# Kernel tuning notes

Hardware: AMD Instinct MI355X
Metric: run time of the kernel (lower is better)

The kernel has to match this reference:

```python
import jax, jax.numpy as jnp
import numpy as np
import math

EMBED = 1024
HEADS = 16
HEAD_DIM = 64
HIDDEN = 4 * EMBED
EPS = 1e-5


def setup_inputs() -> dict:
    key = jax.random.key(0)
    ks = jax.random.split(key, 12)
    B, T, C = 2, 2048, EMBED
    s = 0.02
    return {
        "x": jax.random.normal(ks[0], (B, T, C), jnp.float32),
        "ln1_g": jnp.ones((C,), jnp.float32),
        "ln1_b": jnp.zeros((C,), jnp.float32),
        "qkv_w": jax.random.normal(ks[1], (C, 3 * C), jnp.float32) * s,
        "qkv_b": jnp.zeros((3 * C,), jnp.float32),
        "out_w": jax.random.normal(ks[2], (C, C), jnp.float32) * s,
        "out_b": jnp.zeros((C,), jnp.float32),
        "ln2_g": jnp.ones((C,), jnp.float32),
        "ln2_b": jnp.zeros((C,), jnp.float32),
        "fc1_w": jax.random.normal(ks[3], (C, HIDDEN), jnp.float32) * s,
        "fc1_b": jnp.zeros((HIDDEN,), jnp.float32),
        "fc2_w": jax.random.normal(ks[4], (HIDDEN, C), jnp.float32) * s,
        "fc2_b": jnp.zeros((C,), jnp.float32),
    }


def _layernorm(x, g, b):
    mu = jnp.mean(x, axis=-1, keepdims=True)
    var = jnp.var(x, axis=-1, keepdims=True)
    return (x - mu) * jax.lax.rsqrt(var + EPS) * g + b


def _attention(x, qkv_w, qkv_b, out_w, out_b):
    B, T, C = x.shape
    qkv = x @ qkv_w + qkv_b  # [B,T,3C]
    q, k, v = jnp.split(qkv, 3, axis=-1)
    # [B,H,T,hd]
    def heads(t):
        return t.reshape(B, T, HEADS, HEAD_DIM).transpose(0, 2, 1, 3)
    q, k, v = heads(q), heads(k), heads(v)
    scale = 1.0 / math.sqrt(HEAD_DIM)
    attn = jnp.einsum('bhqd,bhkd->bhqk', q, k) * scale
    causal = jnp.triu(jnp.ones((T, T), bool), k=1)
    attn = jnp.where(causal, -jnp.inf, attn)
    attn = jax.nn.softmax(attn, axis=-1)
    out = jnp.einsum('bhqk,bhkd->bhqd', attn, v)
    out = out.transpose(0, 2, 1, 3).reshape(B, T, C)
    return out @ out_w + out_b


def reference(x, ln1_g, ln1_b, qkv_w, qkv_b, out_w, out_b, ln2_g, ln2_b, fc1_w, fc1_b, fc2_w, fc2_b):
    x = x + _attention(_layernorm(x, ln1_g, ln1_b), qkv_w, qkv_b, out_w, out_b)
    h = _layernorm(x, ln2_g, ln2_b)
    h = jax.nn.gelu(h @ fc1_w + fc1_b, approximate=False) @ fc2_w + fc2_b
    return x + h
```

## Files before the change

### kernel.cpp

```cpp
#include <hip/hip_runtime.h>
#include <hip/hip_bf16.h>
#include <math.h>

typedef float f32x4 __attribute__((ext_vector_type(4)));
typedef __bf16 bf16x8 __attribute__((ext_vector_type(8)));
typedef __hip_bfloat16 bf16;

constexpr int T_SEQ = 2048;
constexpr int C_EMB = 1024;
constexpr int N_HEAD = 16;
constexpr int D_HEAD = 64;
constexpr int BATCH = 2;
constexpr int M_ROWS = BATCH * T_SEQ;
constexpr int HIDDEN_DIM = 4096;

static __device__ __forceinline__ f32x4 zero4() {
  f32x4 z; z[0] = 0.f; z[1] = 0.f; z[2] = 0.f; z[3] = 0.f; return z;
}

static __device__ __forceinline__ void gl_lds16(const bf16* g, bf16* l) {
  __builtin_amdgcn_global_load_lds(
      (const __attribute__((address_space(1))) unsigned int*)g,
      (__attribute__((address_space(3))) unsigned int*)l, 16, 0, 0);
}

static __device__ __forceinline__ int swz_row(int l) {
  return 2 * (l >> 3) + (((l >> 2) ^ (l >> 5)) & 1);
}
static __device__ __forceinline__ int swz_col16(int l) {
  return (l & 3) ^ ((l >> 3) & 3);
}
static __device__ __forceinline__ int swz_rd(int rr, int g) {
  return (rr >> 1) * 64 + ((((rr & 1) ^ ((rr >> 3) & 1))) << 5) +
         (((g ^ ((rr >> 1) & 3)) & 3) << 3);
}

__global__ __launch_bounds__(256) void ln_kernel(const float* __restrict__ x,
                                                 const float* __restrict__ gamma,
                                                 const float* __restrict__ beta,
                                                 bf16* __restrict__ out) {
  int row = blockIdx.x;
  const float* xr = x + (size_t)row * C_EMB;
  int t = threadIdx.x;
  float4 v = *(const float4*)&xr[t * 4];
  float s = v.x + v.y + v.z + v.w;
  float ss = v.x * v.x + v.y * v.y + v.z * v.z + v.w * v.w;
#pragma unroll
  for (int off = 32; off > 0; off >>= 1) {
    s += __shfl_down(s, off, 64);
    ss += __shfl_down(ss, off, 64);
  }
  __shared__ float sbuf[8];
  int w = t >> 6;
  if ((t & 63) == 0) { sbuf[w] = s; sbuf[4 + w] = ss; }
  __syncthreads();
  s = sbuf[0] + sbuf[1] + sbuf[2] + sbuf[3];
  ss = sbuf[4] + sbuf[5] + sbuf[6] + sbuf[7];
  float mu = s * (1.0f / C_EMB);
  float var = ss * (1.0f / C_EMB) - mu * mu;
  float rstd = rsqrtf(var + 1e-5f);
  float4 g4 = *(const float4*)&gamma[t * 4];
  float4 b4 = *(const float4*)&beta[t * 4];
  bf16* orow = out + (size_t)row * C_EMB + t * 4;
  orow[0] = __float2bfloat16((v.x - mu) * rstd * g4.x + b4.x);
  orow[1] = __float2bfloat16((v.y - mu) * rstd * g4.y + b4.y);
  orow[2] = __float2bfloat16((v.z - mu) * rstd * g4.z + b4.z);
  orow[3] = __float2bfloat16((v.w - mu) * rstd * g4.w + b4.w);
}

__global__ __launch_bounds__(256) void cast_transpose(const float* __restrict__ src,
                                                      bf16* __restrict__ dst,
                                                      int K, int N) {
  __shared__ float tile[32][33];
  int n0 = blockIdx.x * 32, k0 = blockIdx.y * 32;
  int tx = threadIdx.x & 31, ty = threadIdx.x >> 5;
#pragma unroll
  for (int i = 0; i < 4; ++i)
    tile[ty + 8 * i][tx] = src[(size_t)(k0 + ty + 8 * i) * N + n0 + tx];
  __syncthreads();
#pragma unroll
  for (int i = 0; i < 4; ++i)
    dst[(size_t)(n0 + ty + 8 * i) * K + k0 + tx] = __float2bfloat16(tile[tx][ty + 8 * i]);
}

__global__ __launch_bounds__(256) void transpose_v(const bf16* __restrict__ V,
                                                   bf16* __restrict__ Vt) {
  int tt = blockIdx.x, bh = blockIdx.y;
  __shared__ bf16 tile[64][72];
  const bf16* src = V + ((size_t)bh * T_SEQ + tt * 64) * 64;
  int t = threadIdx.x;
  for (int idx = t; idx < 512; idx += 256) {
    int r = idx >> 3, c = (idx & 7) * 8;
    *(int4*)&tile[r][c] = *(const int4*)&src[r * 64 + c];
  }
  __syncthreads();
  bf16* dst = Vt + ((size_t)bh * 64) * T_SEQ + tt * 64;
  for (int idx = t; idx < 512; idx += 256) {
    int d = idx >> 3, c = (idx & 7) * 8;
    union { bf16 h[8]; int4 v; } u;
#pragma unroll
    for (int j = 0; j < 8; ++j) u.h[j] = tile[c + j][d];
    *(int4*)&dst[(size_t)d * T_SEQ + c] = u.v;
  }
}

template <int EPI>
__global__ __launch_bounds__(256) void gemm128(
    const bf16* __restrict__ A, const bf16* __restrict__ Bt,
    const float* __restrict__ bias, int M, int N, int K, int ksplit,
    float* __restrict__ out_f32, const float* __restrict__ res,
    bf16* __restrict__ out_b16,
    bf16* __restrict__ q_out, bf16* __restrict__ k_out, bf16* __restrict__ v_out,
    float* __restrict__ part0, float* __restrict__ part1) {
  __shared__ bf16 Alds[2][128 * 32];
  __shared__ bf16 Blds[2][128 * 32];

  int gx = gridDim.x, nwg = gx * gridDim.y;
  int flat = blockIdx.y * gx + blockIdx.x;
  int swz = (flat & 7) * (nwg >> 3) + (flat >> 3);
  int bx = swz % gx, by = swz / gx;

  int m0 = by * 128, n0 = bx * 128;
  int t = threadIdx.x;
  int w = t >> 6, lane = t & 63, g = lane >> 4, r16 = lane & 15;
  int w_m = (w >> 1) * 64, w_n = (w & 1) * 64;

  f32x4 acc[4][4];
#pragma unroll
  for (int i = 0; i < 4; ++i)
#pragma unroll
    for (int j = 0; j < 4; ++j) acc[i][j] = zero4();

  int srow = swz_row(lane);
  int scol = swz_col16(lane) * 8;
  int chunk0 = w * 2, chunk1 = w * 2 + 1;

  int klen = K / ksplit;
  int kbeg = blockIdx.z * klen;
  int NT = klen / 32;

  const bf16* gA0 = A + (size_t)(m0 + chunk0 * 16 + srow) * K + kbeg + scol;
  const bf16* gA1 = A + (size_t)(m0 + chunk1 * 16 + srow) * K + kbeg + scol;
  const bf16* gB0 = Bt + (size_t)(n0 + chunk0 * 16 + srow) * K + kbeg + scol;
  const bf16* gB1 = Bt + (size_t)(n0 + chunk1 * 16 + srow) * K + kbeg + scol;

  int offA[4], offB[4];
#pragma unroll
  for (int mi = 0; mi < 4; ++mi) {
    int R = w_m + mi * 16 + r16;
    offA[mi] = (R >> 4) * 512 + swz_rd(R & 15, g);
  }
#pragma unroll
  for (int ni = 0; ni < 4; ++ni) {
    int R = w_n + ni * 16 + r16;
    offB[ni] = (R >> 4) * 512 + swz_rd(R & 15, g);
  }

  gl_lds16(gA0, &Alds[0][chunk0 * 512]); gA0 += 32;
  gl_lds16(gA1, &Alds[0][chunk1 * 512]); gA1 += 32;
  gl_lds16(gB0, &Blds[0][chunk0 * 512]); gB0 += 32;
  gl_lds16(gB1, &Blds[0][chunk1 * 512]); gB1 += 32;
  __syncthreads();

  for (int tt = 0; tt < NT; ++tt) {
    int cur = tt & 1;
    if (tt + 1 < NT) {
      int nxt = cur ^ 1;
      gl_lds16(gA0, &Alds[nxt][chunk0 * 512]); gA0 += 32;
      gl_lds16(gA1, &Alds[nxt][chunk1 * 512]); gA1 += 32;
      gl_lds16(gB0, &Blds[nxt][chunk0 * 512]); gB0 += 32;
      gl_lds16(gB1, &Blds[nxt][chunk1 * 512]); gB1 += 32;
    }
    bf16x8 af[4], bfr[4];
#pragma unroll
    for (int mi = 0; mi < 4; ++mi)
      af[mi] = *(const bf16x8*)&Alds[cur][offA[mi]];
#pragma unroll
    for (int ni = 0; ni < 4; ++ni)
      bfr[ni] = *(const bf16x8*)&Blds[cur][offB[ni]];
#pragma unroll
    for (int mi = 0; mi < 4; ++mi)
#pragma unroll
      for (int ni = 0; ni < 4; ++ni)
        acc[mi][ni] = __builtin_amdgcn_mfma_f32_16x16x32_bf16(af[mi], bfr[ni], acc[mi][ni], 0, 0, 0);
    __syncthreads();
  }

  float* pout = (EPI == 3) ? (blockIdx.z == 0 ? part0 : part1) : out_f32;

#pragma unroll
  for (int mi = 0; mi < 4; ++mi) {
#pragma unroll
    for (int ni = 0; ni < 4; ++ni) {
      int col = n0 + w_n + ni * 16 + r16;
      float bv = (EPI == 3) ? 0.0f : bias[col];
#pragma unroll
      for (int reg = 0; reg < 4; ++reg) {
        int row = m0 + w_m + mi * 16 + g * 4 + reg;
        float v = acc[mi][ni][reg] + bv;
        if constexpr (EPI == 0) {
          int part = col >> 10, cc = col & 1023;
          int hh = cc >> 6, dd = cc & 63;
          int bb = row >> 11, tt2 = row & 2047;
          size_t idx = (((size_t)bb * N_HEAD + hh) * T_SEQ + tt2) * D_HEAD + dd;
          if (part == 0) q_out[idx] = __float2bfloat16(v * 0.125f);
          else if (part == 1) k_out[idx] = __float2bfloat16(v);
          else v_out[idx] = __float2bfloat16(v);
        } else if constexpr (EPI == 1) {
          size_t idx = (size_t)row * N + col;
          out_f32[idx] = v + res[idx];
        } else if constexpr (EPI == 2) {
          float ge = 0.5f * v * (1.0f + erff(v * 0.70710678118f));
          out_b16[(size_t)row * N + col] = __float2bfloat16(ge);
        } else {
          pout[(size_t)row * N + col] = v;
        }
      }
    }
  }
}

__global__ __launch_bounds__(256) void reduce_add(const float* __restrict__ p0,
                                                  const float* __restrict__ p1,
                                                  const float* __restrict__ bias,
                                                  const float* __restrict__ res,
                                                  float* __restrict__ out,
                                                  int total, int N) {
  for (int i = (blockIdx.x * 256 + threadIdx.x) * 4; i < total; i += gridDim.x * 1024) {
    float4 a = *(const float4*)&p0[i];
    float4 b = *(const float4*)&p1[i];
    float4 r = *(const float4*)&res[i];
    float4 bi = *(const float4*)&bias[i & (N - 1)];
    float4 o;
    o.x = a.x + b.x + r.x + bi.x;
    o.y = a.y + b.y + r.y + bi.y;
    o.z = a.z + b.z + r.z + bi.z;
    o.w = a.w + b.w + r.w + bi.w;
    *(float4*)&out[i] = o;
  }
}

__global__ __launch_bounds__(256) void attn_kernel(const bf16* __restrict__ Q,
                                                   const bf16* __restrict__ Kg,
                                                   const bf16* __restrict__ Vt,
                                                   bf16* __restrict__ O) {
  constexpr int NQ = T_SEQ / 64;
  int p = blockIdx.x, bh = blockIdx.y;
  int qtA = p, qtB = NQ - 1 - p;
  int b = bh >> 4, h = bh & 15;
  __shared__ bf16 Ks[2][64 * 64];
  __shared__ bf16 Vs[2][64 * 64];
  __shared__ bf16 Ps[4][16 * 64];
  int t = threadIdx.x, w = t >> 6, lane = t & 63, g = lane >> 4, r16 = lane & 15;

  const bf16* QpA = Q + ((size_t)bh * T_SEQ + qtA * 64) * 64;
  const bf16* QpB = Q + ((size_t)bh * T_SEQ + qtB * 64) * 64;
  bf16x8 qfA[2], qfB[2];
#pragma unroll
  for (int kk = 0; kk < 2; ++kk) {
    qfA[kk] = *(const bf16x8*)&QpA[(w * 16 + r16) * 64 + kk * 32 + g * 8];
    qfB[kk] = *(const bf16x8*)&QpB[(w * 16 + r16) * 64 + kk * 32 + g * 8];
  }

  float lsA[4] = {0.f, 0.f, 0.f, 0.f}, lsB[4] = {0.f, 0.f, 0.f, 0.f};
  f32x4 oA[4], oB[4];
#pragma unroll
  for (int i = 0; i < 4; ++i) { oA[i] = zero4(); oB[i] = zero4(); }

  bf16* Psw = Ps[w];

  int sg0 = w * 128 + lane, sg1 = w * 128 + 64 + lane;
  int sr0 = sg0 >> 3, sc0 = (sg0 & 7) ^ (sr0 & 7);
  int sr1 = sg1 >> 3, sc1 = (sg1 & 7) ^ (sr1 & 7);

  auto stage = [&](int kt, int buf) {
    const bf16* Kp = Kg + ((size_t)bh * T_SEQ + kt * 64) * 64;
    const bf16* Vp = Vt + (size_t)bh * 64 * T_SEQ + kt * 64;
    gl_lds16(Kp + sr0 * 64 + sc0 * 8, &Ks[buf][(w * 128) * 8]);
    gl_lds16(Vp + (size_t)sr0 * T_SEQ + sc0 * 8, &Vs[buf][(w * 128) * 8]);
    gl_lds16(Kp + sr1 * 64 + sc1 * 8, &Ks[buf][(w * 128 + 64) * 8]);
    gl_lds16(Vp + (size_t)sr1 * T_SEQ + sc1 * 8, &Vs[buf][(w * 128 + 64) * 8]);
  };

  auto process = [&](const bf16x8* qf, float* ls, f32x4* o_acc, bool diag,
                     const bf16* Ksb, const bf16* Vsb) {
    f32x4 s[4];
#pragma unroll
    for (int ni = 0; ni < 4; ++ni) {
      s[ni] = zero4();
#pragma unroll
      for (int kk = 0; kk < 2; ++kk) {
        bf16x8 kf = *(const bf16x8*)&Ksb[(ni * 16 + r16) * 64 + (((kk * 4 + g) ^ (r16 & 7)) << 3)];
        s[ni] = __builtin_amdgcn_mfma_f32_16x16x32_bf16(qf[kk], kf, s[ni], 0, 0, 0);
      }
    }
    if (diag) {
#pragma unroll
      for (int ni = 0; ni < 4; ++ni) {
        int kl = ni * 16 + r16;
#pragma unroll
        for (int reg = 0; reg < 4; ++reg) {
          int ql = w * 16 + g * 4 + reg;
          if (kl > ql) s[ni][reg] = -1e30f;
        }
      }
    }
#pragma unroll
    for (int ni = 0; ni < 4; ++ni) {
#pragma unroll
      for (int reg = 0; reg < 4; ++reg) {
        float pv = __expf(s[ni][reg]);
        s[ni][reg] = pv;
        ls[reg] += pv;
        int rr = g * 4 + reg;
        Psw[rr * 64 + (((ni * 2 + (r16 >> 3)) ^ (rr & 7)) << 3) + (r16 & 7)] =
            __float2bfloat16(pv);
      }
    }
    bf16x8 pf[2];
#pragma unroll
    for (int kk = 0; kk < 2; ++kk)
      pf[kk] = *(const bf16x8*)&Psw[r16 * 64 + (((kk * 4 + g) ^ (r16 & 7)) << 3)];
#pragma unroll
    for (int nd = 0; nd < 4; ++nd)
#pragma unroll
      for (int kk = 0; kk < 2; ++kk) {
        bf16x8 vf = *(const bf16x8*)&Vsb[(nd * 16 + r16) * 64 + (((kk * 4 + g) ^ (r16 & 7)) << 3)];
        o_acc[nd] = __builtin_amdgcn_mfma_f32_16x16x32_bf16(pf[kk], vf, o_acc[nd], 0, 0, 0);
      }
  };

  stage(0, 0);
  __syncthreads();
  for (int kt = 0; kt <= qtB; ++kt) {
    int cur = kt & 1;
    if (kt + 1 <= qtB) stage(kt + 1, cur ^ 1);
    process(qfB, lsB, oB, kt == qtB, &Ks[cur][0], &Vs[cur][0]);
    if (kt <= qtA) process(qfA, lsA, oA, kt == qtA, &Ks[cur][0], &Vs[cur][0]);
    __syncthreads();
  }

#pragma unroll
  for (int reg = 0; reg < 4; ++reg) {
#pragma unroll
    for (int off = 1; off < 16; off <<= 1) {
      lsA[reg] += __shfl_xor(lsA[reg], off, 64);
      lsB[reg] += __shfl_xor(lsB[reg], off, 64);
    }
  }
#pragma unroll
  for (int reg = 0; reg < 4; ++reg) {
    float invA = 1.0f / lsA[reg];
    float invB = 1.0f / lsB[reg];
    int rowA = b * T_SEQ + qtA * 64 + w * 16 + g * 4 + reg;
    int rowB = b * T_SEQ + qtB * 64 + w * 16 + g * 4 + reg;
#pragma unroll
    for (int nd = 0; nd < 4; ++nd) {
      int col = h * 64 + nd * 16 + r16;
      O[(size_t)rowA * C_EMB + col] = __float2bfloat16(oA[nd][reg] * invA);
      O[(size_t)rowB * C_EMB + col] = __float2bfloat16(oB[nd][reg] * invB);
    }
  }
}

extern "C" void kernel_launch(void* const* d_in, const int* in_sizes, int n_in,
                              void* d_out, int out_size, void* d_ws, size_t ws_size,
                              hipStream_t stream) {
  (void)in_sizes; (void)n_in; (void)out_size; (void)ws_size;
  const float* x     = (const float*)d_in[0];
  const float* ln1_g = (const float*)d_in[1];
  const float* ln1_b = (const float*)d_in[2];
  const float* qkv_w = (const float*)d_in[3];
  const float* qkv_b = (const float*)d_in[4];
  const float* out_w = (const float*)d_in[5];
  const float* out_b = (const float*)d_in[6];
  const float* ln2_g = (const float*)d_in[7];
  const float* ln2_b = (const float*)d_in[8];
  const float* fc1_w = (const float*)d_in[9];
  const float* fc1_b = (const float*)d_in[10];
  const float* fc2_w = (const float*)d_in[11];
  const float* fc2_b = (const float*)d_in[12];
  float* out = (float*)d_out;

  char* ws = (char*)d_ws;
  size_t off = 0;
  auto alloc = [&](size_t bytes) {
    void* p = ws + off;
    off += (bytes + 255) & ~(size_t)255;
    return p;
  };
  bf16* Wqkv = (bf16*)alloc((size_t)3 * C_EMB * C_EMB * 2);
  bf16* Wout = (bf16*)alloc((size_t)C_EMB * C_EMB * 2);
  bf16* W1   = (bf16*)alloc((size_t)HIDDEN_DIM * C_EMB * 2);
  bf16* W2   = (bf16*)alloc((size_t)C_EMB * HIDDEN_DIM * 2);
  float* x2  = (float*)alloc((size_t)M_ROWS * C_EMB * 4);
  bf16* Xb   = (bf16*)alloc((size_t)M_ROWS * C_EMB * 2);
  bf16* Qb   = (bf16*)alloc((size_t)M_ROWS * C_EMB * 2 * 4);
  bf16* Kb   = Qb + (size_t)M_ROWS * C_EMB;
  bf16* Vb   = Kb + (size_t)M_ROWS * C_EMB;
  bf16* Vtb  = Vb + (size_t)M_ROWS * C_EMB;
  bf16* H1   = Qb;
  float* p0o = (float*)Qb;
  float* p1o = (float*)Vb;
  float* p0f = (float*)Wqkv;
  float* p1f = (float*)alloc((size_t)M_ROWS * C_EMB * 4);

  cast_transpose<<<dim3(3 * C_EMB / 32, C_EMB / 32), 256, 0, stream>>>(qkv_w, Wqkv, C_EMB, 3 * C_EMB);
  cast_transpose<<<dim3(C_EMB / 32, C_EMB / 32), 256, 0, stream>>>(out_w, Wout, C_EMB, C_EMB);
  cast_transpose<<<dim3(HIDDEN_DIM / 32, C_EMB / 32), 256, 0, stream>>>(fc1_w, W1, C_EMB, HIDDEN_DIM);
  cast_transpose<<<dim3(C_EMB / 32, HIDDEN_DIM / 32), 256, 0, stream>>>(fc2_w, W2, HIDDEN_DIM, C_EMB);

  ln_kernel<<<M_ROWS, 256, 0, stream>>>(x, ln1_g, ln1_b, Xb);

  gemm128<0><<<dim3(3 * C_EMB / 128, M_ROWS / 128), 256, 0, stream>>>(
      Xb, Wqkv, qkv_b, M_ROWS, 3 * C_EMB, C_EMB, 1,
      nullptr, nullptr, nullptr, Qb, Kb, Vb, nullptr, nullptr);

  transpose_v<<<dim3(T_SEQ / 64, BATCH * N_HEAD), 256, 0, stream>>>(Vb, Vtb);

  attn_kernel<<<dim3(T_SEQ / 128, BATCH * N_HEAD), 256, 0, stream>>>(Qb, Kb, Vtb, Xb);

  gemm128<3><<<dim3(C_EMB / 128, M_ROWS / 128, 2), 256, 0, stream>>>(
      Xb, Wout, nullptr, M_ROWS, C_EMB, C_EMB, 2,
      nullptr, nullptr, nullptr, nullptr, nullptr, nullptr, p0o, p1o);
  reduce_add<<<2048, 256, 0, stream>>>(p0o, p1o, out_b, x, x2,
                                       M_ROWS * C_EMB, C_EMB);

  ln_kernel<<<M_ROWS, 256, 0, stream>>>(x2, ln2_g, ln2_b, Xb);

  gemm128<2><<<dim3(HIDDEN_DIM / 128, M_ROWS / 128), 256, 0, stream>>>(
      Xb, W1, fc1_b, M_ROWS, HIDDEN_DIM, C_EMB, 1,
      nullptr, nullptr, H1, nullptr, nullptr, nullptr, nullptr, nullptr);

  gemm128<3><<<dim3(C_EMB / 128, M_ROWS / 128, 2), 256, 0, stream>>>(
      H1, W2, nullptr, M_ROWS, C_EMB, HIDDEN_DIM, 2,
      nullptr, nullptr, nullptr, nullptr, nullptr, nullptr, p0f, p1f);
  reduce_add<<<2048, 256, 0, stream>>>(p0f, p1f, fc2_b, x2, out,
                                       M_ROWS * C_EMB, C_EMB);
}
```

Before: 268.1 us.

## Switch GEMMs to 256-row tiles with 512 threads and fuse residual-add into LayerNorm

Replaces the 128x128, BK=32 GEMM with a 256xBN tile (BN of 256 or 128), 8 waves, BK=64 and a new XOR-swizzled LDS layout. A fragments are software-prefetched in the inner loop. The aim is more data reuse per LDS load and fewer barriers per unit of work. In exchange, each block uses much more LDS (up to 128KB) and the grids become smaller (192–256 blocks), so occupancy drops and CUs may be underfilled. Separately, the split-K reduce plus bias plus residual after the output projection is fused with the second LayerNorm into one kernel, removing one pass over the activations.

```diff
diff --git a/kernel.cpp b/kernel.cpp
--- a/kernel.cpp
+++ b/kernel.cpp
@@ -22,17 +22,6 @@
   __builtin_amdgcn_global_load_lds(
       (const __attribute__((address_space(1))) unsigned int*)g,
       (__attribute__((address_space(3))) unsigned int*)l, 16, 0, 0);
-}
-
-static __device__ __forceinline__ int swz_row(int l) {
-  return 2 * (l >> 3) + (((l >> 2) ^ (l >> 5)) & 1);
-}
-static __device__ __forceinline__ int swz_col16(int l) {
-  return (l & 3) ^ ((l >> 3) & 3);
-}
-static __device__ __forceinline__ int swz_rd(int rr, int g) {
-  return (rr >> 1) * 64 + ((((rr & 1) ^ ((rr >> 3) & 1))) << 5) +
-         (((g ^ ((rr >> 1) & 3)) & 3) << 3);
 }
 
 __global__ __launch_bounds__(256) void ln_kernel(const float* __restrict__ x,
@@ -68,6 +57,52 @@
   orow[3] = __float2bfloat16((v.w - mu) * rstd * g4.w + b4.w);
 }
 
+__global__ __launch_bounds__(256) void ln_red(const float* __restrict__ p0,
+                                              const float* __restrict__ p1,
+                                              const float* __restrict__ bias,
+                                              const float* __restrict__ res,
+                                              const float* __restrict__ gamma,
+                                              const float* __restrict__ beta,
+                                              float* __restrict__ x2,
+                                              bf16* __restrict__ xb) {
+  int row = blockIdx.x;
+  int t = threadIdx.x;
+  size_t base = (size_t)row * C_EMB + t * 4;
+  float4 a = *(const float4*)&p0[base];
+  float4 b = *(const float4*)&p1[base];
+  float4 r = *(const float4*)&res[base];
+  float4 bi = *(const float4*)&bias[t * 4];
+  float4 v;
+  v.x = a.x + b.x + r.x + bi.x;
+  v.y = a.y + b.y + r.y + bi.y;
+  v.z = a.z + b.z + r.z + bi.z;
+  v.w = a.w + b.w + r.w + bi.w;
+  *(float4*)&x2[base] = v;
+  float s = v.x + v.y + v.z + v.w;
+  float ss = v.x * v.x + v.y * v.y + v.z * v.z + v.w * v.w;
+#pragma unroll
+  for (int off = 32; off > 0; off >>= 1) {
+    s += __shfl_down(s, off, 64);
+    ss += __shfl_down(ss, off, 64);
+  }
+  __shared__ float sbuf[8];
+  int w = t >> 6;
+  if ((t & 63) == 0) { sbuf[w] = s; sbuf[4 + w] = ss; }
+  __syncthreads();
+  s = sbuf[0] + sbuf[1] + sbuf[2] + sbuf[3];
+  ss = sbuf[4] + sbuf[5] + sbuf[6] + sbuf[7];
+  float mu = s * (1.0f / C_EMB);
+  float var = ss * (1.0f / C_EMB) - mu * mu;
+  float rstd = rsqrtf(var + 1e-5f);
+  float4 g4 = *(const float4*)&gamma[t * 4];
+  float4 b4 = *(const float4*)&beta[t * 4];
+  bf16* orow = xb + base;
+  orow[0] = __float2bfloat16((v.x - mu) * rstd * g4.x + b4.x);
+  orow[1] = __float2bfloat16((v.y - mu) * rstd * g4.y + b4.y);
+  orow[2] = __float2bfloat16((v.z - mu) * rstd * g4.z + b4.z);
+  orow[3] = __float2bfloat16((v.w - mu) * rstd * g4.w + b4.w);
+}
+
 __global__ __launch_bounds__(256) void cast_transpose(const float* __restrict__ src,
                                                       bf16* __restrict__ dst,
                                                       int K, int N) {
@@ -104,99 +139,118 @@
   }
 }
 
-template <int EPI>
-__global__ __launch_bounds__(256) void gemm128(
+template <int EPI, int BN>
+__global__ __launch_bounds__(512) void gemm256(
     const bf16* __restrict__ A, const bf16* __restrict__ Bt,
     const float* __restrict__ bias, int M, int N, int K, int ksplit,
-    float* __restrict__ out_f32, const float* __restrict__ res,
     bf16* __restrict__ out_b16,
     bf16* __restrict__ q_out, bf16* __restrict__ k_out, bf16* __restrict__ v_out,
     float* __restrict__ part0, float* __restrict__ part1) {
-  __shared__ bf16 Alds[2][128 * 32];
-  __shared__ bf16 Blds[2][128 * 32];
+  constexpr int NFR = BN / 64;
+  constexpr int NB = BN / 64;
+  __shared__ bf16 Abuf[2][256 * 64];
+  __shared__ bf16 Bbuf[2][BN * 64];
 
   int gx = gridDim.x, nwg = gx * gridDim.y;
   int flat = blockIdx.y * gx + blockIdx.x;
   int swz = (flat & 7) * (nwg >> 3) + (flat >> 3);
   int bx = swz % gx, by = swz / gx;
 
-  int m0 = by * 128, n0 = bx * 128;
+  int m0 = by * 256, n0 = bx * BN;
   int t = threadIdx.x;
-  int w = t >> 6, lane = t & 63, g = lane >> 4, r16 = lane & 15;
-  int w_m = (w >> 1) * 64, w_n = (w & 1) * 64;
-
-  f32x4 acc[4][4];
-#pragma unroll
-  for (int i = 0; i < 4; ++i)
-#pragma unroll
-    for (int j = 0; j < 4; ++j) acc[i][j] = zero4();
-
-  int srow = swz_row(lane);
-  int scol = swz_col16(lane) * 8;
-  int chunk0 = w * 2, chunk1 = w * 2 + 1;
+  int wv = t >> 6, lane = t & 63, g = lane >> 4, r16 = lane & 15;
+  int wm = wv >> 2, wn = wv & 3;
+
+  f32x4 acc[8][NFR];
+#pragma unroll
+  for (int i = 0; i < 8; ++i)
+#pragma unroll
+    for (int j = 0; j < NFR; ++j) acc[i][j] = zero4();
+
+  int srow = wv * 8 + (lane >> 3);
+  int srcg = (lane & 7) ^ (lane >> 3);
 
   int klen = K / ksplit;
   int kbeg = blockIdx.z * klen;
-  int NT = klen / 32;
-
-  const bf16* gA0 = A + (size_t)(m0 + chunk0 * 16 + srow) * K + kbeg + scol;
-  const bf16* gA1 = A + (size_t)(m0 + chunk1 * 16 + srow) * K + kbeg + scol;
-  const bf16* gB0 = Bt + (size_t)(n0 + chunk0 * 16 + srow) * K + kbeg + scol;
-  const bf16* gB1 = Bt + (size_t)(n0 + chunk1 * 16 + srow) * K + kbeg + scol;
-
-  int offA[4], offB[4];
-#pragma unroll
-  for (int mi = 0; mi < 4; ++mi) {
-    int R = w_m + mi * 16 + r16;
-    offA[mi] = (R >> 4) * 512 + swz_rd(R & 15, g);
-  }
-#pragma unroll
-  for (int ni = 0; ni < 4; ++ni) {
-    int R = w_n + ni * 16 + r16;
-    offB[ni] = (R >> 4) * 512 + swz_rd(R & 15, g);
-  }
-
-  gl_lds16(gA0, &Alds[0][chunk0 * 512]); gA0 += 32;
-  gl_lds16(gA1, &Alds[0][chunk1 * 512]); gA1 += 32;
-  gl_lds16(gB0, &Blds[0][chunk0 * 512]); gB0 += 32;
-  gl_lds16(gB1, &Blds[0][chunk1 * 512]); gB1 += 32;
-  __syncthreads();
-
+  int NT = klen / 64;
+
+  const bf16* gAp[4];
+  const bf16* gBp[NB];
+#pragma unroll
+  for (int i = 0; i < 4; ++i)
+    gAp[i] = A + (size_t)(m0 + i * 64 + srow) * K + kbeg + srcg * 8;
+#pragma unroll
+  for (int i = 0; i < NB; ++i)
+    gBp[i] = Bt + (size_t)(n0 + i * 64 + srow) * K + kbeg + srcg * 8;
+
+  int aoff[8], boff[NFR], xk[2];
+#pragma unroll
+  for (int mi = 0; mi < 8; ++mi) aoff[mi] = (wm * 128 + mi * 16 + r16) * 64;
+#pragma unroll
+  for (int ni = 0; ni < NFR; ++ni) boff[ni] = (wn * NFR * 16 + ni * 16 + r16) * 64;
+#pragma unroll
+  for (int kk = 0; kk < 2; ++kk) xk[kk] = (((kk * 4 + g) ^ (r16 & 7)) << 3);
+
+  auto stage = [&](int buf) {
+#pragma unroll
+    for (int i = 0; i < 4; ++i) {
+      gl_lds16(gAp[i], &Abuf[buf][(i * 64 + wv * 8) * 64]);
+      gAp[i] += 64;
+    }
+#pragma unroll
+    for (int i = 0; i < NB; ++i) {
+      gl_lds16(gBp[i], &Bbuf[buf][(i * 64 + wv * 8) * 64]);
+      gBp[i] += 64;
+    }
+  };
+
+  auto compute = [&](int buf) {
+    const bf16* Ab = &Abuf[buf][0];
+    const bf16* Bb = &Bbuf[buf][0];
+    bf16x8 bfr[NFR][2];
+#pragma unroll
+    for (int ni = 0; ni < NFR; ++ni)
+#pragma unroll
+      for (int kk = 0; kk < 2; ++kk)
+        bfr[ni][kk] = *(const bf16x8*)&Bb[boff[ni] + xk[kk]];
+    bf16x8 aa[2][2];
+#pragma unroll
+    for (int kk = 0; kk < 2; ++kk) aa[0][kk] = *(const bf16x8*)&Ab[aoff[0] + xk[kk]];
+#pragma unroll
+    for (int mi = 0; mi < 8; ++mi) {
+      if (mi + 1 < 8) {
+#pragma unroll
+        for (int kk = 0; kk < 2; ++kk)
+          aa[(mi + 1) & 1][kk] = *(const bf16x8*)&Ab[aoff[mi + 1] + xk[kk]];
+      }
+#pragma unroll
+      for (int ni = 0; ni < NFR; ++ni) {
+        acc[mi][ni] = __builtin_amdgcn_mfma_f32_16x16x32_bf16(aa[mi & 1][0], bfr[ni][0], acc[mi][ni], 0, 0, 0);
+        acc[mi][ni] = __builtin_amdgcn_mfma_f32_16x16x32_bf16(aa[mi & 1][1], bfr[ni][1], acc[mi][ni], 0, 0, 0);
+      }
+    }
+  };
+
+  stage(0);
+  __syncthreads();
   for (int tt = 0; tt < NT; ++tt) {
     int cur = tt & 1;
-    if (tt + 1 < NT) {
-      int nxt = cur ^ 1;
-      gl_lds16(gA0, &Alds[nxt][chunk0 * 512]); gA0 += 32;
-      gl_lds16(gA1, &Alds[nxt][chunk1 * 512]); gA1 += 32;
-      gl_lds16(gB0, &Blds[nxt][chunk0 * 512]); gB0 += 32;
-      gl_lds16(gB1, &Blds[nxt][chunk1 * 512]); gB1 += 32;
-    }
-    bf16x8 af[4], bfr[4];
-#pragma unroll
-    for (int mi = 0; mi < 4; ++mi)
-      af[mi] = *(const bf16x8*)&Alds[cur][offA[mi]];
-#pragma unroll
-    for (int ni = 0; ni < 4; ++ni)
-      bfr[ni] = *(const bf16x8*)&Blds[cur][offB[ni]];
-#pragma unroll
-    for (int mi = 0; mi < 4; ++mi)
-#pragma unroll
-      for (int ni = 0; ni < 4; ++ni)
-        acc[mi][ni] = __builtin_amdgcn_mfma_f32_16x16x32_bf16(af[mi], bfr[ni], acc[mi][ni], 0, 0, 0);
+    if (tt + 1 < NT) stage(cur ^ 1);
+    compute(cur);
     __syncthreads();
   }
 
-  float* pout = (EPI == 3) ? (blockIdx.z == 0 ? part0 : part1) : out_f32;
-
-#pragma unroll
-  for (int mi = 0; mi < 4; ++mi) {
-#pragma unroll
-    for (int ni = 0; ni < 4; ++ni) {
-      int col = n0 + w_n + ni * 16 + r16;
+  float* pout = (EPI == 3) ? (blockIdx.z == 0 ? part0 : part1) : nullptr;
+
+#pragma unroll
+  for (int mi = 0; mi < 8; ++mi) {
+#pragma unroll
+    for (int ni = 0; ni < NFR; ++ni) {
+      int col = n0 + wn * NFR * 16 + ni * 16 + r16;
       float bv = (EPI == 3) ? 0.0f : bias[col];
 #pragma unroll
       for (int reg = 0; reg < 4; ++reg) {
-        int row = m0 + w_m + mi * 16 + g * 4 + reg;
+        int row = m0 + wm * 128 + mi * 16 + g * 4 + reg;
         float v = acc[mi][ni][reg] + bv;
         if constexpr (EPI == 0) {
           int part = col >> 10, cc = col & 1023;
@@ -206,9 +260,6 @@
           if (part == 0) q_out[idx] = __float2bfloat16(v * 0.125f);
           else if (part == 1) k_out[idx] = __float2bfloat16(v);
           else v_out[idx] = __float2bfloat16(v);
-        } else if constexpr (EPI == 1) {
-          size_t idx = (size_t)row * N + col;
-          out_f32[idx] = v + res[idx];
         } else if constexpr (EPI == 2) {
           float ge = 0.5f * v * (1.0f + erff(v * 0.70710678118f));
           out_b16[(size_t)row * N + col] = __float2bfloat16(ge);
@@ -412,29 +463,26 @@
 
   ln_kernel<<<M_ROWS, 256, 0, stream>>>(x, ln1_g, ln1_b, Xb);
 
-  gemm128<0><<<dim3(3 * C_EMB / 128, M_ROWS / 128), 256, 0, stream>>>(
+  gemm256<0, 256><<<dim3(3 * C_EMB / 256, M_ROWS / 256), 512, 0, stream>>>(
       Xb, Wqkv, qkv_b, M_ROWS, 3 * C_EMB, C_EMB, 1,
-      nullptr, nullptr, nullptr, Qb, Kb, Vb, nullptr, nullptr);
+      nullptr, Qb, Kb, Vb, nullptr, nullptr);
 
   transpose_v<<<dim3(T_SEQ / 64, BATCH * N_HEAD), 256, 0, stream>>>(Vb, Vtb);
 
   attn_kernel<<<dim3(T_SEQ / 128, BATCH * N_HEAD), 256, 0, stream>>>(Qb, Kb, Vtb, Xb);
 
-  gemm128<3><<<dim3(C_EMB / 128, M_ROWS / 128, 2), 256, 0, stream>>>(
+  gemm256<3, 128><<<dim3(C_EMB / 128, M_ROWS / 256, 2), 512, 0, stream>>>(
       Xb, Wout, nullptr, M_ROWS, C_EMB, C_EMB, 2,
-      nullptr, nullptr, nullptr, nullptr, nullptr, nullptr, p0o, p1o);
-  reduce_add<<<2048, 256, 0, stream>>>(p0o, p1o, out_b, x, x2,
-                                       M_ROWS * C_EMB, C_EMB);
-
-  ln_kernel<<<M_ROWS, 256, 0, stream>>>(x2, ln2_g, ln2_b, Xb);
-
-  gemm128<2><<<dim3(HIDDEN_DIM / 128, M_ROWS / 128), 256, 0, stream>>>(
+      nullptr, nullptr, nullptr, nullptr, p0o, p1o);
+  ln_red<<<M_ROWS, 256, 0, stream>>>(p0o, p1o, out_b, x, ln2_g, ln2_b, x2, Xb);
+
+  gemm256<2, 256><<<dim3(HIDDEN_DIM / 256, M_ROWS / 256), 512, 0, stream>>>(
       Xb, W1, fc1_b, M_ROWS, HIDDEN_DIM, C_EMB, 1,
-      nullptr, nullptr, H1, nullptr, nullptr, nullptr, nullptr, nullptr);
-
-  gemm128<3><<<dim3(C_EMB / 128, M_ROWS / 128, 2), 256, 0, stream>>>(
+      H1, nullptr, nullptr, nullptr, nullptr, nullptr);
+
+  gemm256<3, 128><<<dim3(C_EMB / 128, M_ROWS / 256, 2), 512, 0, stream>>>(
       H1, W2, nullptr, M_ROWS, C_EMB, HIDDEN_DIM, 2,
-      nullptr, nullptr, nullptr, nullptr, nullptr, nullptr, p0f, p1f);
+      nullptr, nullptr, nullptr, nullptr, p0f, p1f);
   reduce_add<<<2048, 256, 0, stream>>>(p0f, p1f, fc2_b, x2, out,
                                        M_ROWS * C_EMB, C_EMB);
 }
```

Result: faster. 243.7 us (-9.1%).
